# Kernel optimization log

Hardware: AMD Instinct MI355X
Metric: run time of the kernel (lower is better)

The kernel has to match this reference:

```python
import jax, jax.numpy as jnp
import numpy as np

PHI = 1.618033988749895  # golden ratio
TWO_PI = 2.0 * np.pi
LUT_SIZE = 4096
ALPHA = 1.0


def _wrap(t):
    # wrap_time_periodic: wrap phase into [0, 2*pi)
    return jnp.mod(t, TWO_PI)


def _make_lut():
    ang = (TWO_PI / LUT_SIZE) * jnp.arange(LUT_SIZE, dtype=jnp.float32)
    return jnp.sin(ang), jnp.cos(ang)


def _lut_sin_cos(theta, sin_t, cos_t):
    # 4096-entry LUT sin/cos: quantize wrapped phase to table index
    idx = jnp.floor(_wrap(theta) * (LUT_SIZE / TWO_PI)).astype(jnp.int32) % LUT_SIZE
    return sin_t[idx], cos_t[idx]


def setup_inputs() -> dict:
    key = jax.random.key(0)
    ks = jax.random.split(key, 9)
    B, S, D, N, L, V, SIG = 128, 1024, 256, 1024, 2, 32000, 256
    return {
        "input_ids": jax.random.randint(ks[0], (B, S), 0, V),
        "token_emb": jax.random.normal(ks[1], (V, 2 * D), dtype=jnp.float32) * 0.01,
        "win_r": jax.random.normal(ks[2], (L, D, N), dtype=jnp.float32) / np.sqrt(D),
        "win_i": jax.random.normal(ks[3], (L, D, N), dtype=jnp.float32) / np.sqrt(D),
        "wout_r": jax.random.normal(ks[4], (L, N, D), dtype=jnp.float32) / np.sqrt(N),
        "wout_i": jax.random.normal(ks[5], (L, N, D), dtype=jnp.float32) / np.sqrt(N),
        "omega": jax.random.normal(ks[6], (L, N), dtype=jnp.float32),
        "outp_r": jax.random.normal(ks[7], (D, SIG), dtype=jnp.float32) / np.sqrt(D),
        "outp_i": jax.random.normal(ks[8], (D, SIG), dtype=jnp.float32) / np.sqrt(D),
    }


def reference(input_ids, token_emb, win_r, win_i, wout_r, wout_i, omega, outp_r, outp_i):
    sin_t, cos_t = _make_lut()
    B, S = input_ids.shape
    D = token_emb.shape[1] // 2
    L, N = omega.shape

    emb = token_emb[input_ids]                      # [B, S, 2D]
    w_seq = jnp.transpose(emb[..., :D], (1, 0, 2))  # [S, B, D] time-major
    b_seq = jnp.transpose(emb[..., D:], (1, 0, 2))  # [S, B, D]
    t_seq = jnp.arange(S, dtype=jnp.float32)

    h0 = jnp.zeros((B, D), jnp.float32)
    s0 = jnp.zeros((L, B, N), jnp.float32)

    def step(carry, xs):
        h_r, h_i, s_r, s_i, _, _ = carry
        w, b, t = xs
        # euler_transform: LUT-based complex rotation, no residuals
        wavelength = 1.0 + jnp.abs(w)
        t_phi = _wrap(t * PHI)
        th_r = h_r / wavelength + b + t_phi
        th_i = h_i / wavelength + b + t_phi
        sr, cr = _lut_sin_cos(th_r, sin_t, cos_t)
        si, ci = _lut_sin_cos(th_i, sin_t, cos_t)
        h_r_new = cr * ci - sr * si
        h_i_new = cr * si + sr * ci
        x_r, x_i = h_r_new, h_i_new
        srs, sis = [], []
        for l in range(L):  # small fixed layer loop
            # complex projection into echo chamber
            u_r = x_r @ win_r[l] - x_i @ win_i[l]
            u_i = x_r @ win_i[l] + x_i @ win_r[l]
            # rotate reservoir state by per-neuron frequency + PHI time phase
            sn, cn = _lut_sin_cos(omega[l] + t * PHI, sin_t, cos_t)
            nr = ALPHA * (s_r[l] * cn - s_i[l] * sn) + u_r
            ni = ALPHA * (s_r[l] * sn + s_i[l] * cn) + u_i
            # complex projection back to d_model
            x_r = nr @ wout_r[l] - ni @ wout_i[l]
            x_i = nr @ wout_i[l] + ni @ wout_r[l]
            srs.append(nr)
            sis.append(ni)
        return (h_r_new, h_i_new, jnp.stack(srs), jnp.stack(sis), x_r, x_i), None

    carry0 = (h0, h0, s0, s0, h0, h0)
    (_, _, _, _, x_r, x_i), _ = jax.lax.scan(step, carry0, (w_seq, b_seq, t_seq))

    # output_proj: ComplexLinear(d_model, num_signals, bias=False); logits_real + logits_imag
    lr = x_r @ outp_r - x_i @ outp_i
    li = x_r @ outp_i + x_i @ outp_r
    return lr + li
```

## Files before the change

### kernel.cpp

```cpp
#include <hip/hip_runtime.h>

#define S_LEN 1024
#define BB 128
#define DD 256
#define NN 1024
#define TWO_K 512
#define TWO_N 2048

typedef _Float16 half8 __attribute__((ext_vector_type(8)));
typedef _Float16 half4 __attribute__((ext_vector_type(4)));
typedef float f32x4 __attribute__((ext_vector_type(4)));

__device__ __forceinline__ float wrap2pi(float x) {
  float r = fmodf(x, 6.283185307179586f);
  if (r < 0.f) r += 6.283185307179586f;
  return r;
}
__device__ __forceinline__ int lut_index(float th) {
  float w = wrap2pi(th);
  return ((int)floorf(w * 651.8986469044033f)) & 4095;
}
__device__ __forceinline__ float q12(float th) {
  const float y = floorf(th * 651.8986469044033f) * 0.000244140625f;
  return y - floorf(y);
}

__global__ __launch_bounds__(256) void k_h(const int* __restrict__ ids,
                                           const float* __restrict__ emb,
                                           float* __restrict__ hstate,
                                           _Float16* __restrict__ X0,
                                           int t0, int CH) {
  __shared__ __align__(16) float ebuf[2][8][2][256];
  __shared__ float tphi_s[1024];
  const int tid = threadIdx.x;
  const int lane = tid & 63;
  const int wv = tid >> 6;
  for (int i = tid; i < CH; i += 256)
    tphi_s[i] = wrap2pi((float)(t0 + i) * 1.618033988749895f);

  const int b = blockIdx.x;
  const int d = tid;
  const int* __restrict__ idrow = ids + b * S_LEN + t0;
  const int NST = CH >> 3;

#pragma unroll
  for (int q = 0; q < 2; ++q) {
    const int j = wv * 2 + q;
    const int id = idrow[j];
    const float* src = emb + (size_t)id * 512 + lane * 4;
    __builtin_amdgcn_global_load_lds((const __attribute__((address_space(1))) void*)src,
                                     (__attribute__((address_space(3))) void*)(&ebuf[0][j][0][0]), 16, 0, 0);
    __builtin_amdgcn_global_load_lds((const __attribute__((address_space(1))) void*)(src + 256),
                                     (__attribute__((address_space(3))) void*)(&ebuf[0][j][1][0]), 16, 0, 0);
  }

  float hr, hi;
  if (t0 == 0) { hr = 0.f; hi = 0.f; }
  else { float2 h = ((const float2*)hstate)[b * DD + d]; hr = h.x; hi = h.y; }

  int buf = 0;
  __syncthreads();

  for (int st = 0; st < NST; ++st) {
    if (st + 1 < NST) {
#pragma unroll
      for (int q = 0; q < 2; ++q) {
        const int j = wv * 2 + q;
        const int id = idrow[(st + 1) * 8 + j];
        const float* src = emb + (size_t)id * 512 + lane * 4;
        __builtin_amdgcn_global_load_lds((const __attribute__((address_space(1))) void*)src,
                                         (__attribute__((address_space(3))) void*)(&ebuf[buf ^ 1][j][0][0]), 16, 0, 0);
        __builtin_amdgcn_global_load_lds((const __attribute__((address_space(1))) void*)(src + 256),
                                         (__attribute__((address_space(3))) void*)(&ebuf[buf ^ 1][j][1][0]), 16, 0, 0);
      }
    }
    float rwl[8], bvt[8];
#pragma unroll
    for (int j = 0; j < 8; ++j) {
      const float w  = ebuf[buf][j][0][d];
      const float bv = ebuf[buf][j][1][d];
      rwl[j] = 1.0f / (1.f + fabsf(w));
      bvt[j] = bv + tphi_s[st * 8 + j];
    }
#pragma unroll
    for (int j = 0; j < 8; ++j) {
      const int tt = st * 8 + j;
      const float thr = fmaf(hr, rwl[j], bvt[j]);
      const float thi = fmaf(hi, rwl[j], bvt[j]);
      const float fr = q12(thr);
      const float fi = q12(thi);
      const float sr = __builtin_amdgcn_sinf(fr), cr = __builtin_amdgcn_cosf(fr);
      const float si = __builtin_amdgcn_sinf(fi), ci = __builtin_amdgcn_cosf(fi);
      hr = cr * ci - sr * si;
      hi = cr * si + sr * ci;
      union { unsigned int u; _Float16 h2[2]; } pk;
      pk.h2[0] = (_Float16)hr; pk.h2[1] = (_Float16)hi;
      *(((unsigned int*)(X0 + (size_t)(tt * BB + b) * TWO_K)) + d) = pk.u;
    }
    __syncthreads();
    buf ^= 1;
  }
  ((float2*)hstate)[b * DD + d] = make_float2(hr, hi);
}

__global__ __launch_bounds__(256) void k_rot(const float* __restrict__ omega,
                                             float2* __restrict__ C0, float2* __restrict__ D0,
                                             float2* __restrict__ D1, float2* __restrict__ C1last) {
  const int blk = blockIdx.x;
  const int l = blk >> 10, n = blk & (NN - 1);
  const int tid = threadIdx.x;
  const int lane = tid & 63;
  const int wid = tid >> 6;
  const float om = omega[l * NN + n];

  int pre[4];
  int own = 0;
  const int tb = tid * 4;
#pragma unroll
  for (int j = 0; j < 4; ++j) {
    own += lut_index(om + (float)(tb + j) * 1.618033988749895f);
    pre[j] = own;
  }
  int v = own;
#pragma unroll
  for (int off = 1; off < 64; off <<= 1) {
    int u = __shfl_up(v, off);
    if (lane >= off) v += u;
  }
  __shared__ int wsum[4];
  if (lane == 63) wsum[wid] = v;
  __syncthreads();
  int woff = 0;
#pragma unroll
  for (int w = 0; w < 4; ++w) woff += (w < wid) ? wsum[w] : 0;
  const int excl = woff + v - own;

#pragma unroll
  for (int j = 0; j < 4; ++j) {
    const int t = tb + j;
    const int idx = (excl + pre[j]) & 4095;
    const float s = sinf(0.0015339807878856412f * (float)idx);
    const float c = cosf(0.0015339807878856412f * (float)idx);
    if (l == 0) {
      C0[t * NN + n] = make_float2(c, s);
      D0[t * NN + n] = make_float2(c, -s);
    } else {
      D1[t * NN + n] = make_float2(c, -s);
      if (t == S_LEN - 1) C1last[n] = make_float2(c, s);
    }
  }
}

__global__ __launch_bounds__(256, 2) void k_gemm(const _Float16* __restrict__ A,
                                                 const _Float16* __restrict__ BT,
                                                 _Float16* __restrict__ C,
                                                 int M, int N, int K, int nxlog2,
                                                 const float2* __restrict__ rot) {
  __shared__ __align__(16) _Float16 As[128 * 64];
  __shared__ __align__(16) _Float16 Bs[128 * 64];
  const int tid = threadIdx.x;
  const int lane = tid & 63;
  const int wave = tid >> 6;
  const int wm = wave >> 1;
  const int wn = wave & 1;

  const int cpx = gridDim.x >> 3;
  const int bid = blockIdx.x;
  const int swz = (bid & 7) * cpx + (bid >> 3);
  const int bx = swz & ((1 << nxlog2) - 1);
  const int by = swz >> nxlog2;
  const int m0 = by * 128;
  const int n0 = bx * 128;

  const int srow = lane >> 3;
  const int schunk = (lane & 7) ^ srow;

  f32x4 acc[4][4] = {};

  for (int kt = 0; kt < K; kt += 64) {
#pragma unroll
    for (int j = 0; j < 4; ++j) {
      const int c = wave * 4 + j;
      const int row = c * 8 + srow;
      const _Float16* srcA = A + (size_t)(m0 + row) * K + kt + schunk * 8;
      __builtin_amdgcn_global_load_lds((const __attribute__((address_space(1))) void*)srcA,
                                       (__attribute__((address_space(3))) void*)(As + c * 512), 16, 0, 0);
      const _Float16* srcB = BT + (size_t)(n0 + row) * K + kt + schunk * 8;
      __builtin_amdgcn_global_load_lds((const __attribute__((address_space(1))) void*)srcB,
                                       (__attribute__((address_space(3))) void*)(Bs + c * 512), 16, 0, 0);
    }
    __syncthreads();
#pragma unroll
    for (int ks = 0; ks < 2; ++ks) {
      half8 af[4], bf[4];
#pragma unroll
      for (int mr = 0; mr < 4; ++mr) {
        const int ar = wm * 64 + mr * 16 + (lane & 15);
        const int p = ((ks * 4) + (lane >> 4)) ^ (ar & 7);
        af[mr] = *(const half8*)(As + ar * 64 + p * 8);
      }
#pragma unroll
      for (int nr = 0; nr < 4; ++nr) {
        const int br = wn * 64 + nr * 16 + (lane & 15);
        const int p = ((ks * 4) + (lane >> 4)) ^ (br & 7);
        bf[nr] = *(const half8*)(Bs + br * 64 + p * 8);
      }
#pragma unroll
      for (int mr = 0; mr < 4; ++mr)
#pragma unroll
        for (int nr = 0; nr < 4; ++nr)
          acc[mr][nr] = __builtin_amdgcn_mfma_f32_16x16x32_f16(af[mr], bf[nr], acc[mr][nr], 0, 0, 0);
    }
    __syncthreads();
  }

  const int halfN = N >> 1;
  const int t = by;
#pragma unroll
  for (int mr = 0; mr < 4; ++mr)
#pragma unroll
    for (int nr = 0; nr < 4; ++nr) {
      const int col = n0 + wn * 64 + nr * 16 + (lane & 15);
      const int rbase = m0 + wm * 64 + mr * 16 + ((lane >> 4) << 2);
      float2 dr = make_float2(1.f, 0.f);
      if (rot) dr = rot[(size_t)t * halfN + (col >> 1)];
#pragma unroll
      for (int j = 0; j < 4; ++j) {
        float v = acc[mr][nr][j];
        if (rot) {
          const float pv = __shfl_xor(v, 1);
          v = (lane & 1) ? (dr.x * v + dr.y * pv) : (dr.x * v - dr.y * pv);
        }
        C[(size_t)(rbase + j) * N + col] = (_Float16)v;
      }
    }
}

#define SUF 8
__global__ __launch_bounds__(256) void k_scan(_Float16* __restrict__ V,
                                              const float2* __restrict__ C0c,
                                              float2* __restrict__ ZS, int CH, int first) {
  const int gid = blockIdx.x * 256 + threadIdx.x;
  const int npair = gid & (NN / 2 - 1);
  const int b = gid >> 9;
  const int n = npair * 2;
  float zr0, zi0, zr1, zi1;
  if (first) { zr0 = zi0 = zr1 = zi1 = 0.f; }
  else {
    float4 z = *(const float4*)(ZS + (size_t)b * NN + n);
    zr0 = z.x; zi0 = z.y; zr1 = z.z; zi1 = z.w;
  }
  uint2 vb[SUF], vn[SUF];
  float4 cb[SUF], cn[SUF];
#pragma unroll
  for (int j = 0; j < SUF; ++j) {
    vb[j] = *(const uint2*)(((const unsigned int*)(V + (size_t)(j * BB + b) * TWO_N)) + n);
    cb[j] = *(const float4*)(C0c + (size_t)j * NN + n);
  }
  for (int st = 0; st < CH; st += SUF) {
    const bool more = (st + SUF) < CH;
    if (more) {
#pragma unroll
      for (int j = 0; j < SUF; ++j) {
        vn[j] = *(const uint2*)(((const unsigned int*)(V + (size_t)((st + SUF + j) * BB + b) * TWO_N)) + n);
        cn[j] = *(const float4*)(C0c + (size_t)(st + SUF + j) * NN + n);
      }
    }
#pragma unroll
    for (int j = 0; j < SUF; ++j) {
      union { unsigned int u; _Float16 h2[2]; } a, c;
      a.u = vb[j].x; c.u = vb[j].y;
      zr0 += (float)a.h2[0]; zi0 += (float)a.h2[1];
      zr1 += (float)c.h2[0]; zi1 += (float)c.h2[1];
      const float4 cc = cb[j];
      a.h2[0] = (_Float16)(cc.x * zr0 - cc.y * zi0);
      a.h2[1] = (_Float16)(cc.x * zi0 + cc.y * zr0);
      c.h2[0] = (_Float16)(cc.z * zr1 - cc.w * zi1);
      c.h2[1] = (_Float16)(cc.z * zi1 + cc.w * zr1);
      *(uint2*)(((unsigned int*)(V + (size_t)((st + j) * BB + b) * TWO_N)) + n) = make_uint2(a.u, c.u);
    }
#pragma unroll
    for (int j = 0; j < SUF; ++j) { vb[j] = vn[j]; cb[j] = cn[j]; }
  }
  *(float4*)(ZS + (size_t)b * NN + n) = make_float4(zr0, zi0, zr1, zi1);
}

__global__ __launch_bounds__(256) void k_reduce(const _Float16* __restrict__ U,
                                                float* __restrict__ s1, int CH, int first) {
  const int gid = blockIdx.x * 256 + threadIdx.x;
  const int g = gid & (TWO_N / 4 - 1);
  const int b = gid >> 9;
  const int np = g * 4;
  f32x4 acc;
  if (first) {
#pragma unroll
    for (int j = 0; j < 4; ++j) acc[j] = 0.f;
  } else {
    acc = *(const f32x4*)(s1 + (size_t)b * TWO_N + np);
  }
  half4 vb[SUF], vn[SUF];
#pragma unroll
  for (int j = 0; j < SUF; ++j)
    vb[j] = *(const half4*)(U + (size_t)(j * BB + b) * TWO_N + np);
  for (int st = 0; st < CH; st += SUF) {
    const bool more = (st + SUF) < CH;
    if (more) {
#pragma unroll
      for (int j = 0; j < SUF; ++j)
        vn[j] = *(const half4*)(U + (size_t)((st + SUF + j) * BB + b) * TWO_N + np);
    }
#pragma unroll
    for (int j = 0; j < SUF; ++j) {
#pragma unroll
      for (int q = 0; q < 4; ++q) acc[q] += (float)vb[j][q];
    }
#pragma unroll
    for (int j = 0; j < SUF; ++j) vb[j] = vn[j];
  }
  *(f32x4*)(s1 + (size_t)b * TWO_N + np) = acc;
}

__global__ __launch_bounds__(256) void k_tail1(const float* __restrict__ s1,
                                               const float2* __restrict__ C1last,
                                               const float* __restrict__ BT,
                                               float* __restrict__ C) {
  const int wave = threadIdx.x >> 6;
  const int lane = threadIdx.x & 63;
  const int o = blockIdx.x * 4 + wave;
  const int row = o >> 9;
  const int col = o & (TWO_K - 1);
  const float4* __restrict__ a4 = (const float4*)(s1 + (size_t)row * TWO_N);
  const float4* __restrict__ c4 = (const float4*)C1last;
  const float4* __restrict__ b4 = (const float4*)(BT + (size_t)col * TWO_N);
  float acc = 0.f;
#pragma unroll
  for (int it = 0; it < 8; ++it) {
    const int idx = it * 64 + lane;
    const float4 av = a4[idx];
    const float4 cc = c4[idx];
    const float4 bv = b4[idx];
    const float r0 = cc.x * av.x - cc.y * av.y;
    const float i0 = cc.x * av.y + cc.y * av.x;
    const float r1 = cc.z * av.z - cc.w * av.w;
    const float i1 = cc.z * av.w + cc.w * av.z;
    acc = fmaf(r0, bv.x, acc);
    acc = fmaf(i0, bv.y, acc);
    acc = fmaf(r1, bv.z, acc);
    acc = fmaf(i1, bv.w, acc);
  }
#pragma unroll
  for (int s = 32; s >= 1; s >>= 1) acc += __shfl_xor(acc, s);
  if (lane == 0) C[o] = acc;
}

__global__ __launch_bounds__(256) void k_tail(const float* __restrict__ A,
                                              const float* __restrict__ BT,
                                              float* __restrict__ C, int M, int N, int K) {
  const int wave = threadIdx.x >> 6;
  const int lane = threadIdx.x & 63;
  const int o = blockIdx.x * 4 + wave;
  if (o >= M * N) return;
  const int row = o / N;
  const int col = o - row * N;
  const float4* __restrict__ a4 = (const float4*)(A + (size_t)row * K);
  const float4* __restrict__ b4 = (const float4*)(BT + (size_t)col * K);
  float acc = 0.f;
  const int nit = K >> 8;
  for (int it = 0; it < nit; ++it) {
    const float4 av = a4[it * 64 + lane];
    const float4 bv = b4[it * 64 + lane];
    acc = fmaf(av.x, bv.x, acc);
    acc = fmaf(av.y, bv.y, acc);
    acc = fmaf(av.z, bv.z, acc);
    acc = fmaf(av.w, bv.w, acc);
  }
#pragma unroll
  for (int s = 32; s >= 1; s >>= 1) acc += __shfl_xor(acc, s);
  if (lane == 0) C[o] = acc;
}

__global__ __launch_bounds__(256) void k_prep_in(const float* __restrict__ r, const float* __restrict__ im,
                                                 _Float16* __restrict__ dst) {
  const int gid = blockIdx.x * 256 + threadIdx.x;
  const int n = gid & (NN - 1);
  const int k = gid >> 10;
  const float rv = r[(size_t)k * NN + n], iv = im[(size_t)k * NN + n];
  const size_t base = (size_t)(2 * n) * TWO_K + 2 * k;
  dst[base] = (_Float16)rv;              dst[base + 1] = (_Float16)(-iv);
  dst[base + TWO_K] = (_Float16)iv;      dst[base + TWO_K + 1] = (_Float16)rv;
}
__global__ __launch_bounds__(256) void k_prep_out(const float* __restrict__ r, const float* __restrict__ im,
                                                  _Float16* __restrict__ dst) {
  const int gid = blockIdx.x * 256 + threadIdx.x;
  const int d = gid & (DD - 1);
  const int n = gid >> 8;
  const float rv = r[(size_t)n * DD + d], iv = im[(size_t)n * DD + d];
  const size_t base = (size_t)(2 * d) * TWO_N + 2 * n;
  dst[base] = (_Float16)rv;              dst[base + 1] = (_Float16)(-iv);
  dst[base + TWO_N] = (_Float16)iv;      dst[base + TWO_N + 1] = (_Float16)rv;
}
__global__ __launch_bounds__(256) void k_prep_wout1T(const float* __restrict__ r, const float* __restrict__ im,
                                                     float* __restrict__ dstT) {
  const int gid = blockIdx.x * 256 + threadIdx.x;
  const int n = gid & (NN - 1);
  const int d = gid >> 10;
  const float rv = r[(size_t)n * DD + d], iv = im[(size_t)n * DD + d];
  const size_t b0 = (size_t)(2 * d) * TWO_N + 2 * n;
  const size_t b1 = (size_t)(2 * d + 1) * TWO_N + 2 * n;
  dstT[b0] = rv;     dstT[b0 + 1] = -iv;
  dstT[b1] = iv;     dstT[b1 + 1] = rv;
}
__global__ __launch_bounds__(256) void k_prep_finT(const float* __restrict__ pr, const float* __restrict__ pi_,
                                                   float* __restrict__ dstT) {
  const int gid = blockIdx.x * 256 + threadIdx.x;
  const int d = gid & (DD - 1);
  const int s = gid >> 8;
  const float a = pr[(size_t)d * 256 + s], b = pi_[(size_t)d * 256 + s];
  dstT[(size_t)s * TWO_K + 2 * d] = a + b;
  dstT[(size_t)s * TWO_K + 2 * d + 1] = a - b;
}

extern "C" void kernel_launch(void* const* d_in, const int* in_sizes, int n_in,
                              void* d_out, int out_size, void* d_ws, size_t ws_size,
                              hipStream_t stream) {
  const int* ids      = (const int*)d_in[0];
  const float* emb    = (const float*)d_in[1];
  const float* win_r  = (const float*)d_in[2];
  const float* win_i  = (const float*)d_in[3];
  const float* wout_r = (const float*)d_in[4];
  const float* wout_i = (const float*)d_in[5];
  const float* omega  = (const float*)d_in[6];
  const float* outp_r = (const float*)d_in[7];
  const float* outp_i = (const float*)d_in[8];

  char* ws = (char*)d_ws;
  size_t off = 0;
  auto alloc = [&](size_t bytes) { void* p = ws + off; off += (bytes + 255) & ~(size_t)255; return p; };

  float2* C0     = (float2*)alloc((size_t)S_LEN * NN * 8);
  float2* D0     = (float2*)alloc((size_t)S_LEN * NN * 8);
  float2* D1     = (float2*)alloc((size_t)S_LEN * NN * 8);
  float2* C1last = (float2*)alloc((size_t)NN * 8);
  float2* ZS     = (float2*)alloc((size_t)BB * NN * 8);
  float* hstate  = (float*)alloc((size_t)BB * DD * 2 * 4);
  float* s1      = (float*)alloc((size_t)BB * TWO_N * 4);
  float* xt      = (float*)alloc((size_t)BB * TWO_K * 4);
  _Float16* BTin0  = (_Float16*)alloc((size_t)TWO_N * TWO_K * 2);
  _Float16* BTout0 = (_Float16*)alloc((size_t)TWO_K * TWO_N * 2);
  _Float16* BTin1  = (_Float16*)alloc((size_t)TWO_N * TWO_K * 2);
  float* Wout1T = (float*)alloc((size_t)TWO_K * TWO_N * 4);
  float* WfinT  = (float*)alloc((size_t)256 * TWO_K * 4);
  const size_t fixed = off;

  int CH = 1024;
  while (CH > 32) {
    size_t need = fixed + (size_t)CH * BB * 2 * (TWO_K + TWO_N) + 2 * 256;
    if (need <= ws_size) break;
    CH >>= 1;
  }
  _Float16* X0 = (_Float16*)alloc((size_t)CH * BB * TWO_K * 2);
  _Float16* VB = (_Float16*)alloc((size_t)CH * BB * TWO_N * 2);
  _Float16* Yc = X0;

  k_rot<<<2 * NN, 256, 0, stream>>>(omega, C0, D0, D1, C1last);
  k_prep_in<<<DD * NN / 256, 256, 0, stream>>>(win_r, win_i, BTin0);
  k_prep_in<<<DD * NN / 256, 256, 0, stream>>>(win_r + (size_t)DD * NN, win_i + (size_t)DD * NN, BTin1);
  k_prep_out<<<NN * DD / 256, 256, 0, stream>>>(wout_r, wout_i, BTout0);
  k_prep_wout1T<<<NN * DD / 256, 256, 0, stream>>>(wout_r + (size_t)NN * DD, wout_i + (size_t)NN * DD, Wout1T);
  k_prep_finT<<<DD * 256 / 256, 256, 0, stream>>>(outp_r, outp_i, WfinT);

  const int nchunks = S_LEN / CH;
  for (int c = 0; c < nchunks; ++c) {
    const int t0 = c * CH;
    const int M = CH * BB;
    k_h<<<BB, 256, 0, stream>>>(ids, emb, hstate, X0, t0, CH);
    const int nb1 = (M / 128) * (TWO_N / 128);
    k_gemm<<<nb1, 256, 0, stream>>>(X0, BTin0, VB, M, TWO_N, TWO_K, 4, D0 + (size_t)t0 * NN);
    k_scan<<<BB * (NN / 2) / 256, 256, 0, stream>>>(VB, C0 + (size_t)t0 * NN, ZS, CH, c == 0);
    const int nb2 = (M / 128) * (TWO_K / 128);
    k_gemm<<<nb2, 256, 0, stream>>>(VB, BTout0, Yc, M, TWO_K, TWO_N, 2, nullptr);
    k_gemm<<<nb1, 256, 0, stream>>>(Yc, BTin1, VB, M, TWO_N, TWO_K, 4, D1 + (size_t)t0 * NN);
    k_reduce<<<BB * (TWO_N / 4) / 256, 256, 0, stream>>>(VB, s1, CH, c == 0);
  }

  k_tail1<<<BB * TWO_K / 4, 256, 0, stream>>>(s1, C1last, Wout1T, xt);
  k_tail<<<BB * 256 / 4, 256, 0, stream>>>(xt, WfinT, (float*)d_out, BB, 256, TWO_K);
}
```

Before: 1.653 ms.

## Replace prefix-rotation scaling with direct per-step recurrence in scan and reduce

Layer-0 reservoir scan now uses the per-step rotation directly (z = R_t z + u_t) instead of scaling GEMM outputs by cumulative inverse rotations and multiplying back afterward, which removes the prefix-scan work and the D0 and C0 tables for layer 0. Layer-1's cumulative de-rotation moves from the GEMM epilogue into k_reduce, so every k_gemm launch drops its rotation loads and lane shuffles. The intent is a lighter GEMM epilogue and fewer rotation tables, at the cost of extra FMAs and table loads in the memory-bound reduce kernel. Precision also changes because the fp16 state written out is now the actual reservoir state rather than a rotated one.

```diff
diff --git a/kernel.cpp b/kernel.cpp
--- a/kernel.cpp
+++ b/kernel.cpp
@@ -104,8 +104,8 @@
 }
 
 __global__ __launch_bounds__(256) void k_rot(const float* __restrict__ omega,
-                                             float2* __restrict__ C0, float2* __restrict__ D0,
-                                             float2* __restrict__ D1, float2* __restrict__ C1last) {
+                                             float2* __restrict__ R0, float2* __restrict__ D1,
+                                             float2* __restrict__ C1last) {
   const int blk = blockIdx.x;
   const int l = blk >> 10, n = blk & (NN - 1);
   const int tid = threadIdx.x;
@@ -113,13 +113,24 @@
   const int wid = tid >> 6;
   const float om = omega[l * NN + n];
 
-  int pre[4];
+  int idxv[4], pre[4];
   int own = 0;
   const int tb = tid * 4;
 #pragma unroll
   for (int j = 0; j < 4; ++j) {
-    own += lut_index(om + (float)(tb + j) * 1.618033988749895f);
+    idxv[j] = lut_index(om + (float)(tb + j) * 1.618033988749895f);
+    own += idxv[j];
     pre[j] = own;
+  }
+  if (l == 0) {
+#pragma unroll
+    for (int j = 0; j < 4; ++j) {
+      const int t = tb + j;
+      const float s = sinf(0.0015339807878856412f * (float)idxv[j]);
+      const float c = cosf(0.0015339807878856412f * (float)idxv[j]);
+      R0[t * NN + n] = make_float2(c, s);
+    }
+    return;
   }
   int v = own;
 #pragma unroll
@@ -141,21 +152,15 @@
     const int idx = (excl + pre[j]) & 4095;
     const float s = sinf(0.0015339807878856412f * (float)idx);
     const float c = cosf(0.0015339807878856412f * (float)idx);
-    if (l == 0) {
-      C0[t * NN + n] = make_float2(c, s);
-      D0[t * NN + n] = make_float2(c, -s);
-    } else {
-      D1[t * NN + n] = make_float2(c, -s);
-      if (t == S_LEN - 1) C1last[n] = make_float2(c, s);
-    }
+    D1[t * NN + n] = make_float2(c, -s);
+    if (t == S_LEN - 1) C1last[n] = make_float2(c, s);
   }
 }
 
 __global__ __launch_bounds__(256, 2) void k_gemm(const _Float16* __restrict__ A,
                                                  const _Float16* __restrict__ BT,
                                                  _Float16* __restrict__ C,
-                                                 int M, int N, int K, int nxlog2,
-                                                 const float2* __restrict__ rot) {
+                                                 int M, int N, int K, int nxlog2) {
   __shared__ __align__(16) _Float16 As[128 * 64];
   __shared__ __align__(16) _Float16 Bs[128 * 64];
   const int tid = threadIdx.x;
@@ -214,31 +219,21 @@
     __syncthreads();
   }
 
-  const int halfN = N >> 1;
-  const int t = by;
 #pragma unroll
   for (int mr = 0; mr < 4; ++mr)
 #pragma unroll
     for (int nr = 0; nr < 4; ++nr) {
       const int col = n0 + wn * 64 + nr * 16 + (lane & 15);
       const int rbase = m0 + wm * 64 + mr * 16 + ((lane >> 4) << 2);
-      float2 dr = make_float2(1.f, 0.f);
-      if (rot) dr = rot[(size_t)t * halfN + (col >> 1)];
-#pragma unroll
-      for (int j = 0; j < 4; ++j) {
-        float v = acc[mr][nr][j];
-        if (rot) {
-          const float pv = __shfl_xor(v, 1);
-          v = (lane & 1) ? (dr.x * v + dr.y * pv) : (dr.x * v - dr.y * pv);
-        }
-        C[(size_t)(rbase + j) * N + col] = (_Float16)v;
-      }
+#pragma unroll
+      for (int j = 0; j < 4; ++j)
+        C[(size_t)(rbase + j) * N + col] = (_Float16)acc[mr][nr][j];
     }
 }
 
 #define SUF 8
 __global__ __launch_bounds__(256) void k_scan(_Float16* __restrict__ V,
-                                              const float2* __restrict__ C0c,
+                                              const float2* __restrict__ R0c,
                                               float2* __restrict__ ZS, int CH, int first) {
   const int gid = blockIdx.x * 256 + threadIdx.x;
   const int npair = gid & (NN / 2 - 1);
@@ -250,12 +245,13 @@
     float4 z = *(const float4*)(ZS + (size_t)b * NN + n);
     zr0 = z.x; zi0 = z.y; zr1 = z.z; zi1 = z.w;
   }
+  const float4* __restrict__ r4 = (const float4*)R0c;
   uint2 vb[SUF], vn[SUF];
   float4 cb[SUF], cn[SUF];
 #pragma unroll
   for (int j = 0; j < SUF; ++j) {
     vb[j] = *(const uint2*)(((const unsigned int*)(V + (size_t)(j * BB + b) * TWO_N)) + n);
-    cb[j] = *(const float4*)(C0c + (size_t)j * NN + n);
+    cb[j] = r4[(size_t)j * (NN / 2) + npair];
   }
   for (int st = 0; st < CH; st += SUF) {
     const bool more = (st + SUF) < CH;
@@ -263,20 +259,21 @@
 #pragma unroll
       for (int j = 0; j < SUF; ++j) {
         vn[j] = *(const uint2*)(((const unsigned int*)(V + (size_t)((st + SUF + j) * BB + b) * TWO_N)) + n);
-        cn[j] = *(const float4*)(C0c + (size_t)(st + SUF + j) * NN + n);
+        cn[j] = r4[(size_t)(st + SUF + j) * (NN / 2) + npair];
       }
     }
 #pragma unroll
     for (int j = 0; j < SUF; ++j) {
       union { unsigned int u; _Float16 h2[2]; } a, c;
       a.u = vb[j].x; c.u = vb[j].y;
-      zr0 += (float)a.h2[0]; zi0 += (float)a.h2[1];
-      zr1 += (float)c.h2[0]; zi1 += (float)c.h2[1];
       const float4 cc = cb[j];
-      a.h2[0] = (_Float16)(cc.x * zr0 - cc.y * zi0);
-      a.h2[1] = (_Float16)(cc.x * zi0 + cc.y * zr0);
-      c.h2[0] = (_Float16)(cc.z * zr1 - cc.w * zi1);
-      c.h2[1] = (_Float16)(cc.z * zi1 + cc.w * zr1);
+      const float w0r = cc.x * zr0 - cc.y * zi0 + (float)a.h2[0];
+      const float w0i = cc.x * zi0 + cc.y * zr0 + (float)a.h2[1];
+      const float w1r = cc.z * zr1 - cc.w * zi1 + (float)c.h2[0];
+      const float w1i = cc.z * zi1 + cc.w * zr1 + (float)c.h2[1];
+      zr0 = w0r; zi0 = w0i; zr1 = w1r; zi1 = w1i;
+      a.h2[0] = (_Float16)zr0; a.h2[1] = (_Float16)zi0;
+      c.h2[0] = (_Float16)zr1; c.h2[1] = (_Float16)zi1;
       *(uint2*)(((unsigned int*)(V + (size_t)((st + j) * BB + b) * TWO_N)) + n) = make_uint2(a.u, c.u);
     }
 #pragma unroll
@@ -286,6 +283,7 @@
 }
 
 __global__ __launch_bounds__(256) void k_reduce(const _Float16* __restrict__ U,
+                                                const float2* __restrict__ D1c,
                                                 float* __restrict__ s1, int CH, int first) {
   const int gid = blockIdx.x * 256 + threadIdx.x;
   const int g = gid & (TWO_N / 4 - 1);
@@ -298,24 +296,35 @@
   } else {
     acc = *(const f32x4*)(s1 + (size_t)b * TWO_N + np);
   }
+  const float4* __restrict__ d4 = (const float4*)D1c;
   half4 vb[SUF], vn[SUF];
-#pragma unroll
-  for (int j = 0; j < SUF; ++j)
+  float4 db[SUF], dn[SUF];
+#pragma unroll
+  for (int j = 0; j < SUF; ++j) {
     vb[j] = *(const half4*)(U + (size_t)(j * BB + b) * TWO_N + np);
+    db[j] = d4[(size_t)j * (NN / 2) + g];
+  }
   for (int st = 0; st < CH; st += SUF) {
     const bool more = (st + SUF) < CH;
     if (more) {
 #pragma unroll
-      for (int j = 0; j < SUF; ++j)
+      for (int j = 0; j < SUF; ++j) {
         vn[j] = *(const half4*)(U + (size_t)((st + SUF + j) * BB + b) * TWO_N + np);
+        dn[j] = d4[(size_t)(st + SUF + j) * (NN / 2) + g];
+      }
     }
 #pragma unroll
     for (int j = 0; j < SUF; ++j) {
-#pragma unroll
-      for (int q = 0; q < 4; ++q) acc[q] += (float)vb[j][q];
-    }
-#pragma unroll
-    for (int j = 0; j < SUF; ++j) vb[j] = vn[j];
+      const float u0 = (float)vb[j][0], u1 = (float)vb[j][1];
+      const float u2 = (float)vb[j][2], u3 = (float)vb[j][3];
+      const float4 d = db[j];
+      acc[0] += d.x * u0 - d.y * u1;
+      acc[1] += d.x * u1 + d.y * u0;
+      acc[2] += d.z * u2 - d.w * u3;
+      acc[3] += d.z * u3 + d.w * u2;
+    }
+#pragma unroll
+    for (int j = 0; j < SUF; ++j) { vb[j] = vn[j]; db[j] = dn[j]; }
   }
   *(f32x4*)(s1 + (size_t)b * TWO_N + np) = acc;
 }
@@ -437,8 +446,7 @@
   size_t off = 0;
   auto alloc = [&](size_t bytes) { void* p = ws + off; off += (bytes + 255) & ~(size_t)255; return p; };
 
-  float2* C0     = (float2*)alloc((size_t)S_LEN * NN * 8);
-  float2* D0     = (float2*)alloc((size_t)S_LEN * NN * 8);
+  float2* R0     = (float2*)alloc((size_t)S_LEN * NN * 8);
   float2* D1     = (float2*)alloc((size_t)S_LEN * NN * 8);
   float2* C1last = (float2*)alloc((size_t)NN * 8);
   float2* ZS     = (float2*)alloc((size_t)BB * NN * 8);
@@ -462,7 +470,7 @@
   _Float16* VB = (_Float16*)alloc((size_t)CH * BB * TWO_N * 2);
   _Float16* Yc = X0;
 
-  k_rot<<<2 * NN, 256, 0, stream>>>(omega, C0, D0, D1, C1last);
+  k_rot<<<2 * NN, 256, 0, stream>>>(omega, R0, D1, C1last);
   k_prep_in<<<DD * NN / 256, 256, 0, stream>>>(win_r, win_i, BTin0);
   k_prep_in<<<DD * NN / 256, 256, 0, stream>>>(win_r + (size_t)DD * NN, win_i + (size_t)DD * NN, BTin1);
   k_prep_out<<<NN * DD / 256, 256, 0, stream>>>(wout_r, wout_i, BTout0);
@@ -475,12 +483,12 @@
     const int M = CH * BB;
     k_h<<<BB, 256, 0, stream>>>(ids, emb, hstate, X0, t0, CH);
     const int nb1 = (M / 128) * (TWO_N / 128);
-    k_gemm<<<nb1, 256, 0, stream>>>(X0, BTin0, VB, M, TWO_N, TWO_K, 4, D0 + (size_t)t0 * NN);
-    k_scan<<<BB * (NN / 2) / 256, 256, 0, stream>>>(VB, C0 + (size_t)t0 * NN, ZS, CH, c == 0);
+    k_gemm<<<nb1, 256, 0, stream>>>(X0, BTin0, VB, M, TWO_N, TWO_K, 4);
+    k_scan<<<BB * (NN / 2) / 256, 256, 0, stream>>>(VB, R0 + (size_t)t0 * NN, ZS, CH, c == 0);
     const int nb2 = (M / 128) * (TWO_K / 128);
-    k_gemm<<<nb2, 256, 0, stream>>>(VB, BTout0, Yc, M, TWO_K, TWO_N, 2, nullptr);
-    k_gemm<<<nb1, 256, 0, stream>>>(Yc, BTin1, VB, M, TWO_N, TWO_K, 4, D1 + (size_t)t0 * NN);
-    k_reduce<<<BB * (TWO_N / 4) / 256, 256, 0, stream>>>(VB, s1, CH, c == 0);
+    k_gemm<<<nb2, 256, 0, stream>>>(VB, BTout0, Yc, M, TWO_K, TWO_N, 2);
+    k_gemm<<<nb1, 256, 0, stream>>>(Yc, BTin1, VB, M, TWO_N, TWO_K, 4);
+    k_reduce<<<BB * (TWO_N / 4) / 256, 256, 0, stream>>>(VB, D1 + (size_t)t0 * NN, s1, CH, c == 0);
   }
 
   k_tail1<<<BB * TWO_K / 4, 256, 0, stream>>>(s1, C1last, Wout1T, xt);
```

Measured after the change: 1.492 ms. 9.7% less time.
